# Kernel optimization log

Hardware: AMD Instinct MI355X
Metric: run time of the kernel (lower is better)

## Reference

```python
import jax, jax.numpy as jnp
import numpy as np

B, D, U = 8192, 512, 512


def setup_inputs() -> dict:
    key = jax.random.key(0)
    ks = jax.random.split(key, 5)
    return {
        "inputs": jax.random.normal(ks[0], (B, D), dtype=jnp.float32),
        "h_tm1": jax.random.normal(ks[1], (B, U), dtype=jnp.float32),
        "c_tm1": jax.random.normal(ks[2], (B, U), dtype=jnp.float32),
        "kernel": jax.random.normal(ks[3], (D, 4 * U), dtype=jnp.float32) * (1.0 / np.sqrt(D)),
        "recurrent_kernel": jax.random.normal(ks[4], (U, 4 * U), dtype=jnp.float32) * (1.0 / np.sqrt(U)),
        "bias": jnp.zeros((4 * U,), dtype=jnp.float32),
    }


def reference(inputs, h_tm1, c_tm1, kernel, recurrent_kernel, bias):
    # z: [B, 4U] = x @ W + h @ R + b
    z = inputs @ kernel + h_tm1 @ recurrent_kernel + bias
    z0, z1, z2, z3 = jnp.split(z, 4, axis=1)
    i = jax.nn.sigmoid(z0)
    f = jax.nn.sigmoid(z1)
    g = jnp.tanh(z2)
    o = jax.nn.sigmoid(z3)
    c = f * c_tm1 + i * g
    h = o * jnp.tanh(c)
    return (h, h, c)
```

## Files before the change

kernel.cpp:

```cpp
#include <hip/hip_runtime.h>
#include <hip/hip_bf16.h>
#include <cstdint>
#include <cstddef>

#define BB 8192
#define UU 512
#define KPACK 1024
#define NPACK 2048

using frag16 = __attribute__((ext_vector_type(8))) short;
using f32x4  = __attribute__((ext_vector_type(4))) float;

__device__ inline float fast_sigmoid(float x) {
  float e = __expf(-x);
  return __builtin_amdgcn_rcpf(1.0f + e);
}
__device__ inline float fast_tanh(float x) {
  float e = __expf(-2.0f * x);
  return fmaf(2.0f, __builtin_amdgcn_rcpf(1.0f + e), -1.0f);
}

__device__ inline unsigned cvt2(float lo, float hi) {
  __hip_bfloat162 b = __float22bfloat162_rn(float2{lo, hi});
  union { __hip_bfloat162 b; unsigned u; } v; v.b = b;
  return v.u;
}

__global__ __launch_bounds__(256) void pack_kernel(const float* __restrict__ x,
                                                   const float* __restrict__ h,
                                                   const float* __restrict__ W,
                                                   const float* __restrict__ R,
                                                   short* __restrict__ Xp,
                                                   short* __restrict__ Bt) {
  if (blockIdx.x < 4096) {
    int idx = blockIdx.x * 256 + threadIdx.x;
    int row = idx >> 7;
    int k8  = (idx & 127) << 3;
    const float* src = (k8 < 512) ? (x + (size_t)row * 512 + k8)
                                  : (h + (size_t)row * 512 + (k8 - 512));
    float4 a = *(const float4*)(src);
    float4 b = *(const float4*)(src + 4);
    uint4 o;
    o.x = cvt2(a.x, a.y);
    o.y = cvt2(a.z, a.w);
    o.z = cvt2(b.x, b.y);
    o.w = cvt2(b.z, b.w);
    *(uint4*)(Xp + ((size_t)idx << 3)) = o;
  } else {
    __shared__ float tile[64][65];
    int b2 = blockIdx.x - 4096;
    int nb = (b2 & 31) * 64;
    int kb = (b2 >> 5) * 64;
    int t  = threadIdx.x;
#pragma unroll
    for (int rep = 0; rep < 16; ++rep) {
      int kr = rep * 4 + (t >> 6);
      int c  = t & 63;
      int kg = kb + kr;
      const float* s = (kg < 512) ? (W + (size_t)kg * 2048) : (R + (size_t)(kg - 512) * 2048);
      tile[c][kr] = s[nb + c];
    }
    __syncthreads();
#pragma unroll
    for (int rep = 0; rep < 4; ++rep) {
      int nn = rep * 16 + (t >> 4);
      int k4 = (t & 15) << 2;
      uint2 o;
      o.x = cvt2(tile[nn][k4 + 0], tile[nn][k4 + 1]);
      o.y = cvt2(tile[nn][k4 + 2], tile[nn][k4 + 3]);
      *(uint2*)(Bt + (size_t)(nb + nn) * 1024 + kb + k4) = o;
    }
  }
}

__global__ __launch_bounds__(256, 4) void lstm_mfma_kernel(
    const short* __restrict__ A,
    const short* __restrict__ Bt,
    const float* __restrict__ bias,
    const float* __restrict__ cprev,
    float* __restrict__ out)
{
  __shared__ short lds_a[128 * 64];
  __shared__ short lds_b[128 * 64];

  const int tid  = threadIdx.x;
  const int lane = tid & 63;
  const int wave = tid >> 6;
  const int wm = wave & 1, wn = wave >> 1;
  const int bm = blockIdx.x;
  const int bn = blockIdx.y;

  const int r8  = lane >> 3;
  const int kg  = lane & 7;
  const int kgx = kg ^ r8;

  const short* ga[4];
  const short* gb[4];
  int ls_off[4];
#pragma unroll
  for (int t = 0; t < 4; ++t) {
    int rowl = wave * 32 + t * 8 + r8;
    ga[t] = A + (size_t)(bm * 128 + rowl) * 1024 + kgx * 8;
    int u    = bn * 32 + ((rowl >> 6) << 4) + (rowl & 15);
    int gate = (rowl >> 4) & 3;
    gb[t] = Bt + (size_t)(gate * 512 + u) * 1024 + kgx * 8;
    ls_off[t] = (wave * 32 + t * 8) * 64;
  }

  const int q   = lane >> 4;
  const int c16 = lane & 15;
  const int mx  = c16 & 7;

  f32x4 acc[4][4];
#pragma unroll
  for (int i = 0; i < 4; ++i)
#pragma unroll
    for (int j = 0; j < 4; ++j)
      acc[i][j] = f32x4{0.f, 0.f, 0.f, 0.f};

  for (int kt = 0; kt < 16; ++kt) {
    const int k0 = kt * 64;
#pragma unroll
    for (int t = 0; t < 4; ++t)
      __builtin_amdgcn_global_load_lds(
          (const __attribute__((address_space(1))) void*)(ga[t] + k0),
          (__attribute__((address_space(3))) void*)(lds_a + ls_off[t]), 16, 0, 0);
#pragma unroll
    for (int t = 0; t < 4; ++t)
      __builtin_amdgcn_global_load_lds(
          (const __attribute__((address_space(1))) void*)(gb[t] + k0),
          (__attribute__((address_space(3))) void*)(lds_b + ls_off[t]), 16, 0, 0);
    __syncthreads();
#pragma unroll
    for (int s = 0; s < 2; ++s) {
      const int kch = (((s << 2) + q) ^ mx) << 3;
      frag16 af[4], bf[4];
#pragma unroll
      for (int i = 0; i < 4; ++i)
        af[i] = *(const frag16*)(lds_a + (wm * 64 + i * 16 + c16) * 64 + kch);
#pragma unroll
      for (int j = 0; j < 4; ++j)
        bf[j] = *(const frag16*)(lds_b + (wn * 64 + j * 16 + c16) * 64 + kch);
#pragma unroll
      for (int i = 0; i < 4; ++i)
#pragma unroll
        for (int j = 0; j < 4; ++j)
          acc[i][j] = __builtin_amdgcn_mfma_f32_16x16x32_bf16(af[i], bf[j], acc[i][j], 0, 0, 0);
    }
    __syncthreads();
  }

  const int u = bn * 32 + wn * 16 + c16;
  const float b0 = bias[u];
  const float b1 = bias[512 + u];
  const float b2 = bias[1024 + u];
  const float b3 = bias[1536 + u];
  float* outh0 = out;
  float* outh1 = out + (size_t)BB * UU;
  float* outc  = out + (size_t)2 * BB * UU;

#pragma unroll
  for (int i = 0; i < 4; ++i) {
    int row0 = bm * 128 + wm * 64 + i * 16 + q * 4;
#pragma unroll
    for (int r = 0; r < 4; ++r) {
      size_t off = (size_t)(row0 + r) * UU + u;
      float z0 = acc[i][0][r] + b0;
      float z1 = acc[i][1][r] + b1;
      float z2 = acc[i][2][r] + b2;
      float z3 = acc[i][3][r] + b3;
      float ig = fast_sigmoid(z0);
      float fg = fast_sigmoid(z1);
      float gg = fast_tanh(z2);
      float og = fast_sigmoid(z3);
      float cp = cprev[off];
      float cc = fg * cp + ig * gg;
      float hh = og * fast_tanh(cc);
      outh0[off] = hh;
      outh1[off] = hh;
      outc[off]  = cc;
    }
  }
}

extern "C" void kernel_launch(void* const* d_in, const int* in_sizes, int n_in,
                              void* d_out, int out_size, void* d_ws, size_t ws_size,
                              hipStream_t stream) {
  const float* x  = (const float*)d_in[0];
  const float* h  = (const float*)d_in[1];
  const float* c  = (const float*)d_in[2];
  const float* W  = (const float*)d_in[3];
  const float* R  = (const float*)d_in[4];
  const float* b  = (const float*)d_in[5];
  float* out = (float*)d_out;

  short* Xp = (short*)d_ws;
  short* Bt = Xp + (size_t)BB * KPACK;

  pack_kernel<<<4608, 256, 0, stream>>>(x, h, W, R, Xp, Bt);
  lstm_mfma_kernel<<<dim3(64, 16), 256, 0, stream>>>(Xp, Bt, b, c, out);
}
```

Baseline: 146.9 us.

## Double-buffer A tile in LDS and load B fragments directly from global

The A tile now goes through two LDS buffers, so the next k-tile is prefetched while the current one feeds the MFMAs. This replaces the two syncthreads per iteration with a single wait plus barrier. B fragments are no longer staged in LDS; each wave reads its own B operand straight from global memory into registers. This cuts LDS traffic and sync stalls, but B loads become per-wave global reads that are duplicated across the two M-waves and the 64 bm blocks, relying on cache hits, and they add register pressure.

```diff
diff --git a/kernel.cpp b/kernel.cpp
--- a/kernel.cpp
+++ b/kernel.cpp
@@ -80,8 +80,7 @@
     const float* __restrict__ cprev,
     float* __restrict__ out)
 {
-  __shared__ short lds_a[128 * 64];
-  __shared__ short lds_b[128 * 64];
+  __shared__ short lds_a[2 * 8192];
 
   const int tid  = threadIdx.x;
   const int lane = tid & 63;
@@ -95,15 +94,11 @@
   const int kgx = kg ^ r8;
 
   const short* ga[4];
-  const short* gb[4];
   int ls_off[4];
 #pragma unroll
   for (int t = 0; t < 4; ++t) {
     int rowl = wave * 32 + t * 8 + r8;
     ga[t] = A + (size_t)(bm * 128 + rowl) * 1024 + kgx * 8;
-    int u    = bn * 32 + ((rowl >> 6) << 4) + (rowl & 15);
-    int gate = (rowl >> 4) & 3;
-    gb[t] = Bt + (size_t)(gate * 512 + u) * 1024 + kgx * 8;
     ls_off[t] = (wave * 32 + t * 8) * 64;
   }
 
@@ -111,46 +106,63 @@
   const int c16 = lane & 15;
   const int mx  = c16 & 7;
 
-  f32x4 acc[4][4];
-#pragma unroll
-  for (int i = 0; i < 4; ++i)
-#pragma unroll
-    for (int j = 0; j < 4; ++j)
-      acc[i][j] = f32x4{0.f, 0.f, 0.f, 0.f};
-
-  for (int kt = 0; kt < 16; ++kt) {
+  const int u = bn * 32 + wn * 16 + c16;
+  const short* Bp[4];
+#pragma unroll
+  for (int j = 0; j < 4; ++j)
+    Bp[j] = Bt + (size_t)(j * 512 + u) * 1024 + q * 8;
+
+  auto STAGE = [&](int kt, int bi) {
     const int k0 = kt * 64;
+    short* base = lds_a + bi * 8192;
 #pragma unroll
     for (int t = 0; t < 4; ++t)
       __builtin_amdgcn_global_load_lds(
           (const __attribute__((address_space(1))) void*)(ga[t] + k0),
-          (__attribute__((address_space(3))) void*)(lds_a + ls_off[t]), 16, 0, 0);
-#pragma unroll
-    for (int t = 0; t < 4; ++t)
-      __builtin_amdgcn_global_load_lds(
-          (const __attribute__((address_space(1))) void*)(gb[t] + k0),
-          (__attribute__((address_space(3))) void*)(lds_b + ls_off[t]), 16, 0, 0);
-    __syncthreads();
+          (__attribute__((address_space(3))) void*)(base + ls_off[t]), 16, 0, 0);
+  };
+
+  f32x4 acc[4][4];
+#pragma unroll
+  for (int i = 0; i < 4; ++i)
+#pragma unroll
+    for (int j = 0; j < 4; ++j)
+      acc[i][j] = f32x4{0.f, 0.f, 0.f, 0.f};
+
+  STAGE(0, 0);
+  asm volatile("s_waitcnt vmcnt(0)" ::: "memory");
+  __builtin_amdgcn_s_barrier();
+
+  for (int kt = 0; kt < 16; ++kt) {
+    const short* la = lds_a + (kt & 1) * 8192;
+
+    frag16 bfv[2][4];
+#pragma unroll
+    for (int s = 0; s < 2; ++s)
+#pragma unroll
+      for (int j = 0; j < 4; ++j)
+        bfv[s][j] = *(const frag16*)(Bp[j] + kt * 64 + s * 32);
+
+    if (kt < 15) STAGE(kt + 1, (kt + 1) & 1);
+
 #pragma unroll
     for (int s = 0; s < 2; ++s) {
       const int kch = (((s << 2) + q) ^ mx) << 3;
-      frag16 af[4], bf[4];
+      frag16 af[4];
 #pragma unroll
       for (int i = 0; i < 4; ++i)
-        af[i] = *(const frag16*)(lds_a + (wm * 64 + i * 16 + c16) * 64 + kch);
-#pragma unroll
-      for (int j = 0; j < 4; ++j)
-        bf[j] = *(const frag16*)(lds_b + (wn * 64 + j * 16 + c16) * 64 + kch);
+        af[i] = *(const frag16*)(la + (wm * 64 + i * 16 + c16) * 64 + kch);
 #pragma unroll
       for (int i = 0; i < 4; ++i)
 #pragma unroll
         for (int j = 0; j < 4; ++j)
-          acc[i][j] = __builtin_amdgcn_mfma_f32_16x16x32_bf16(af[i], bf[j], acc[i][j], 0, 0, 0);
-    }
-    __syncthreads();
-  }
-
-  const int u = bn * 32 + wn * 16 + c16;
+          acc[i][j] = __builtin_amdgcn_mfma_f32_16x16x32_bf16(af[i], bfv[s][j], acc[i][j], 0, 0, 0);
+    }
+
+    asm volatile("s_waitcnt vmcnt(0)" ::: "memory");
+    __builtin_amdgcn_s_barrier();
+  }
+
   const float b0 = bias[u];
   const float b1 = bias[512 + u];
   const float b2 = bias[1024 + u];
```

New measurement: 189.7 us. 1.29x slower.

## Switch GEMM to 32x32x16 bf16 MFMA with per-wave 32-row tiles

Applied to the files above, without the earlier changes.

Replaces the 16x16x32 MFMA tiling (each wave computing a 64x64 sub-tile from 4x4 fragments) with 32x32x16 MFMAs, where each wave owns 32 rows and all 128 gate-columns. B-tile rows are remapped so each 32-row group holds one gate, and the epilogue indexing is rewritten for the 32x32 accumulator layout. This cuts LDS fragment reads per MFMA and the instruction count, in exchange for each wave loading every B fragment, which raises LDS traffic for B.

```diff
diff --git a/kernel.cpp b/kernel.cpp
--- a/kernel.cpp
+++ b/kernel.cpp
@@ -10,6 +10,7 @@
 
 using frag16 = __attribute__((ext_vector_type(8))) short;
 using f32x4  = __attribute__((ext_vector_type(4))) float;
+using f32x16 = __attribute__((ext_vector_type(16))) float;
 
 __device__ inline float fast_sigmoid(float x) {
   float e = __expf(-x);
@@ -86,7 +87,6 @@
   const int tid  = threadIdx.x;
   const int lane = tid & 63;
   const int wave = tid >> 6;
-  const int wm = wave & 1, wn = wave >> 1;
   const int bm = blockIdx.x;
   const int bn = blockIdx.y;
 
@@ -101,22 +101,20 @@
   for (int t = 0; t < 4; ++t) {
     int rowl = wave * 32 + t * 8 + r8;
     ga[t] = A + (size_t)(bm * 128 + rowl) * 1024 + kgx * 8;
-    int u    = bn * 32 + ((rowl >> 6) << 4) + (rowl & 15);
-    int gate = (rowl >> 4) & 3;
-    gb[t] = Bt + (size_t)(gate * 512 + u) * 1024 + kgx * 8;
+    int u_b  = bn * 32 + (rowl & 31);
+    int gate = rowl >> 5;
+    gb[t] = Bt + (size_t)(gate * 512 + u_b) * 1024 + kgx * 8;
     ls_off[t] = (wave * 32 + t * 8) * 64;
   }
 
-  const int q   = lane >> 4;
-  const int c16 = lane & 15;
-  const int mx  = c16 & 7;
+  const int l31 = lane & 31;
+  const int q2  = lane >> 5;
+  const int mx8 = lane & 7;
 
-  f32x4 acc[4][4];
+  f32x16 acc[4];
 #pragma unroll
-  for (int i = 0; i < 4; ++i)
-#pragma unroll
-    for (int j = 0; j < 4; ++j)
-      acc[i][j] = f32x4{0.f, 0.f, 0.f, 0.f};
+  for (int j = 0; j < 4; ++j)
+    acc[j] = (f32x16)(0.0f);
 
   for (int kt = 0; kt < 16; ++kt) {
     const int k0 = kt * 64;
@@ -132,25 +130,21 @@
           (__attribute__((address_space(3))) void*)(lds_b + ls_off[t]), 16, 0, 0);
     __syncthreads();
 #pragma unroll
-    for (int s = 0; s < 2; ++s) {
-      const int kch = (((s << 2) + q) ^ mx) << 3;
-      frag16 af[4], bf[4];
-#pragma unroll
-      for (int i = 0; i < 4; ++i)
-        af[i] = *(const frag16*)(lds_a + (wm * 64 + i * 16 + c16) * 64 + kch);
+    for (int s4 = 0; s4 < 4; ++s4) {
+      const int kch = (((s4 << 1) | q2) ^ mx8) << 3;
+      frag16 af = *(const frag16*)(lds_a + (wave * 32 + l31) * 64 + kch);
+      frag16 bfv[4];
 #pragma unroll
       for (int j = 0; j < 4; ++j)
-        bf[j] = *(const frag16*)(lds_b + (wn * 64 + j * 16 + c16) * 64 + kch);
+        bfv[j] = *(const frag16*)(lds_b + (j * 32 + l31) * 64 + kch);
 #pragma unroll
-      for (int i = 0; i < 4; ++i)
-#pragma unroll
-        for (int j = 0; j < 4; ++j)
-          acc[i][j] = __builtin_amdgcn_mfma_f32_16x16x32_bf16(af[i], bf[j], acc[i][j], 0, 0, 0);
+      for (int j = 0; j < 4; ++j)
+        acc[j] = __builtin_amdgcn_mfma_f32_32x32x16_bf16(af, bfv[j], acc[j], 0, 0, 0);
     }
     __syncthreads();
   }
 
-  const int u = bn * 32 + wn * 16 + c16;
+  const int u = bn * 32 + l31;
   const float b0 = bias[u];
   const float b1 = bias[512 + u];
   const float b2 = bias[1024 + u];
@@ -160,15 +154,16 @@
   float* outc  = out + (size_t)2 * BB * UU;
 
 #pragma unroll
-  for (int i = 0; i < 4; ++i) {
-    int row0 = bm * 128 + wm * 64 + i * 16 + q * 4;
+  for (int g = 0; g < 4; ++g) {
 #pragma unroll
-    for (int r = 0; r < 4; ++r) {
-      size_t off = (size_t)(row0 + r) * UU + u;
-      float z0 = acc[i][0][r] + b0;
-      float z1 = acc[i][1][r] + b1;
-      float z2 = acc[i][2][r] + b2;
-      float z3 = acc[i][3][r] + b3;
+    for (int rr = 0; rr < 4; ++rr) {
+      const int r16 = g * 4 + rr;
+      const int row = bm * 128 + wave * 32 + rr + 8 * g + 4 * q2;
+      size_t off = (size_t)row * UU + u;
+      float z0 = acc[0][r16] + b0;
+      float z1 = acc[1][r16] + b1;
+      float z2 = acc[2][r16] + b2;
+      float z3 = acc[3][r16] + b3;
       float ig = fast_sigmoid(z0);
       float fg = fast_sigmoid(z1);
       float gg = fast_tanh(z2);
```

Measured after the change: 150.9 us. +2.7%, slower.
